# Kernel optimization log

Hardware: AMD Instinct MI355X
Metric: run time of the kernel (lower is better)

## Reference

```python
import jax, jax.numpy as jnp
import numpy as np

N = 50000   # nodes
E = 400000  # directed edges (line-graph nodes)
LE = 1600000  # line-graph edges
B = 256     # graphs in batch
F = 64      # n_feats
ED = 16     # edge_dim
NIT = 3     # n_iter
SF = 6 * F  # LinearBlock hidden


def _seg_softmax(vals, seg, num):
    # numerically stable segment softmax (PyG softmax)
    m = jax.ops.segment_max(vals, seg, num_segments=num)
    e = jnp.exp(vals - m[seg])
    s = jax.ops.segment_sum(e, seg, num_segments=num)
    return e / (s[seg] + 1e-16)


def _gat_pool(out, lg_src, lg_dst, batch, gat_W, att_src, att_dst, gat_bias):
    # PyG GATConv(F, 1): heads=1, add_self_loops=True, negative_slope=0.2
    xw = out @ gat_W                       # [E, 1]
    sl = jnp.arange(E, dtype=lg_src.dtype)
    src = jnp.concatenate([lg_src, sl])
    dst = jnp.concatenate([lg_dst, sl])
    a_s = xw[:, 0] * att_src[0]
    a_d = xw[:, 0] * att_dst[0]
    alpha = jax.nn.leaky_relu(a_s[src] + a_d[dst], negative_slope=0.2)
    coef = _seg_softmax(alpha, dst, E)     # softmax over incoming line-edges
    xc = jax.ops.segment_sum(coef[:, None] * xw[src], dst, num_segments=E) + gat_bias  # [E,1]
    # GlobalAttentionPool: segment softmax over batch, then weighted sum pool
    sc = _seg_softmax(xc[:, 0], batch, B)[:, None]
    return jax.ops.segment_sum(out * sc, batch, num_segments=B)  # [B, F]


def _bn(x, g, b):
    # BatchNorm1d in training mode (batch stats, biased var, eps=1e-5)
    m = x.mean(0)
    v = ((x - m) ** 2).mean(0)
    return (x - m) * jax.lax.rsqrt(v + 1e-5) * g + b


def _prelu(x, w):
    return jnp.where(x >= 0, x, w * x)


def _lin_block(x, bn1_g, bn1_b, W1, b1, bn_g, bn_b, pr, W, b, bn5_g, bn5_b, pr5, W5, b5):
    x = _bn(x, bn1_g, bn1_b) @ W1 + b1                       # lin1: [N, 6F]
    h = _prelu(_bn(x, bn_g[0], bn_b[0]), pr[0]) @ W[0] + b[0]  # lin2
    h = _prelu(_bn(h, bn_g[1], bn_b[1]), pr[1]) @ W[1] + b[1]  # lin3
    x = (h + x) / 2
    x = (_prelu(_bn(x, bn_g[2], bn_b[2]), pr[2]) @ W[2] + b[2] + x) / 2  # lin4
    x = _prelu(_bn(x, bn5_g, bn5_b), pr5) @ W5 + b5          # lin5: [N, F]
    return x


def setup_inputs() -> dict:
    key = jax.random.key(0)
    ks = jax.random.split(key, 20)
    def nrm(k, shape, s=0.1):
        return jax.random.normal(k, shape, jnp.float32) * s
    inp = {}
    inp["x"] = jax.random.normal(ks[0], (N, F), jnp.float32)
    inp["edge_attr"] = jax.random.normal(ks[1], (E, ED), jnp.float32)
    inp["edge_index"] = jax.random.randint(ks[2], (2, E), 0, N, jnp.int32)
    inp["line_graph_edge_index"] = jax.random.randint(ks[3], (2, LE), 0, E, jnp.int32)
    inp["edge_index_batch"] = jnp.sort(jax.random.randint(ks[4], (E,), 0, B, jnp.int32))
    inp["W_u"] = nrm(ks[5], (F, F)); inp["W_v"] = nrm(ks[6], (F, F)); inp["W_e"] = nrm(ks[7], (ED, F))
    inp["gat_W"] = nrm(ks[8], (F, 1)); inp["gat_att_src"] = nrm(ks[9], (1,)); inp["gat_att_dst"] = nrm(ks[10], (1,))
    inp["gat_bias"] = jnp.zeros((1,), jnp.float32)
    inp["a"] = nrm(ks[11], (1, F, NIT)); inp["a_bias"] = jnp.zeros((1, 1, NIT), jnp.float32)
    inp["W_gout"] = nrm(ks[12], (F, F)); inp["b_gout"] = jnp.zeros((F,), jnp.float32)
    inp["lb_bn1_g"] = jnp.ones((F,), jnp.float32); inp["lb_bn1_b"] = jnp.zeros((F,), jnp.float32)
    inp["lb_W1"] = nrm(ks[13], (F, SF)); inp["lb_b1"] = jnp.zeros((SF,), jnp.float32)
    inp["lb_bn_g"] = jnp.ones((3, SF), jnp.float32); inp["lb_bn_b"] = jnp.zeros((3, SF), jnp.float32)
    inp["lb_pr"] = jnp.full((3,), 0.25, jnp.float32)
    inp["lb_W"] = nrm(ks[14], (3, SF, SF)); inp["lb_b"] = jnp.zeros((3, SF), jnp.float32)
    inp["lb_bn5_g"] = jnp.ones((SF,), jnp.float32); inp["lb_bn5_b"] = jnp.zeros((SF,), jnp.float32)
    inp["lb_pr5"] = jnp.array(0.25, jnp.float32)
    inp["lb_W5"] = nrm(ks[15], (SF, F)); inp["lb_b5"] = jnp.zeros((F,), jnp.float32)
    return inp


def reference(x, edge_attr, W_u, W_v, W_e, gat_W, gat_att_src, gat_att_dst, gat_bias,
              a, a_bias, W_gout, b_gout,
              lb_bn1_g, lb_bn1_b, lb_W1, lb_b1, lb_bn_g, lb_bn_b, lb_pr, lb_W, lb_b,
              lb_bn5_g, lb_bn5_b, lb_pr5, lb_W5, lb_b5,
              edge_index, line_graph_edge_index, edge_index_batch):
    ei0, ei1 = edge_index[0], edge_index[1]
    lg0, lg1 = line_graph_edge_index[0], line_graph_edge_index[1]
    # initial directed-edge features
    ea = ((x @ W_u)[ei0] + (x @ W_v)[ei1] + edge_attr @ W_e) / 3.0  # [E, F]
    out = ea
    outs, gouts = [], []
    for _ in range(NIT):
        out = ea + jax.ops.segment_sum(out[lg0], lg1, num_segments=E)  # line-graph message passing
        gout = _gat_pool(out, lg0, lg1, edge_index_batch, gat_W, gat_att_src, gat_att_dst, gat_bias)
        outs.append(out)
        gouts.append(jnp.tanh(gout @ W_gout + b_gout))
    out_all = jnp.stack(outs, -1)    # [E, F, NIT]
    gout_all = jnp.stack(gouts, -1)  # [B, F, NIT]
    sc = jax.nn.softmax((gout_all * a).sum(1, keepdims=True) + a_bias, axis=-1)  # [B,1,NIT]
    out = (out_all * sc[edge_index_batch]).sum(-1)  # per-edge gather == repeat_interleave(degree)
    xn = x + jax.ops.segment_sum(out, ei1, num_segments=N)
    return _lin_block(xn, lb_bn1_g, lb_bn1_b, lb_W1, lb_b1, lb_bn_g, lb_bn_b, lb_pr, lb_W, lb_b,
                      lb_bn5_g, lb_bn5_b, lb_pr5, lb_W5, lb_b5)
```

## Files before the change

### kernel.cpp

```cpp
#include <hip/hip_runtime.h>
#include <math.h>

#define NN 50000
#define EE 400000
#define LEE 1600000
#define BBATCH 256
#define FF 64
#define EDD 16
#define NITER 3
#define SFD 384

#define CDIV(a,b) (((a)+(b)-1)/(b))

typedef unsigned short ushort_t;
typedef __attribute__((ext_vector_type(8))) short bf16x8;
typedef __attribute__((ext_vector_type(4))) float f32x4;

__device__ inline float b2f(ushort_t u) { return __uint_as_float(((unsigned)u) << 16); }
__device__ inline ushort_t f2b(float f) {
    unsigned u = __float_as_uint(f);
    return (ushort_t)((u + 0x7fffu + ((u >> 16) & 1u)) >> 16);
}

__global__ void k_hist(const int* __restrict__ idx, int n, int* __restrict__ cnt) {
    int i = blockIdx.x * blockDim.x + threadIdx.x;
    if (i < n) atomicAdd(&cnt[idx[i]], 1);
}
__global__ void k_part(const int* __restrict__ in, int n, int* __restrict__ part) {
    __shared__ int s[256];
    int i = blockIdx.x * 256 + threadIdx.x;
    s[threadIdx.x] = (i < n) ? in[i] : 0;
    __syncthreads();
    for (int off = 128; off > 0; off >>= 1) {
        if (threadIdx.x < off) s[threadIdx.x] += s[threadIdx.x + off];
        __syncthreads();
    }
    if (threadIdx.x == 0) part[blockIdx.x] = s[0];
}
__global__ void k_scan_single(int* __restrict__ a, int n) {
    __shared__ int s[256];
    int v = (threadIdx.x < n) ? a[threadIdx.x] : 0;
    s[threadIdx.x] = v; __syncthreads();
    for (int off = 1; off < 256; off <<= 1) {
        int t = (threadIdx.x >= off) ? s[threadIdx.x - off] : 0;
        __syncthreads(); s[threadIdx.x] += t; __syncthreads();
    }
    if (threadIdx.x < n) a[threadIdx.x] = s[threadIdx.x] - v;
}
__global__ void k_scan_add(int* __restrict__ a, int n, const int* __restrict__ off) {
    __shared__ int s[256];
    int i = blockIdx.x * 256 + threadIdx.x;
    int v = (i < n) ? a[i] : 0;
    s[threadIdx.x] = v; __syncthreads();
    for (int o = 1; o < 256; o <<= 1) {
        int t = (threadIdx.x >= o) ? s[threadIdx.x - o] : 0;
        __syncthreads(); s[threadIdx.x] += t; __syncthreads();
    }
    if (i < n) a[i] = s[threadIdx.x] - v + off[blockIdx.x];
}
__global__ void k_scan_out(const int* __restrict__ in, int n, const int* __restrict__ boff,
                           int* __restrict__ out) {
    __shared__ int s[256];
    int i = blockIdx.x * 256 + threadIdx.x;
    int v = (i < n) ? in[i] : 0;
    s[threadIdx.x] = v; __syncthreads();
    for (int o = 1; o < 256; o <<= 1) {
        int t = (threadIdx.x >= o) ? s[threadIdx.x - o] : 0;
        __syncthreads(); s[threadIdx.x] += t; __syncthreads();
    }
    if (i < n) out[i] = s[threadIdx.x] - v + boff[blockIdx.x];
    if (i == n - 1) out[n] = s[threadIdx.x] + boff[blockIdx.x];
}
__global__ void k_fill_lg(const int* __restrict__ lg, const int* __restrict__ rowptr,
                          int* __restrict__ cnt, int* __restrict__ srcidx) {
    int i = blockIdx.x * blockDim.x + threadIdx.x;
    if (i >= LEE) return;
    int d = lg[LEE + i];
    int pos = rowptr[d] + atomicAdd(&cnt[d], 1);
    srcidx[pos] = lg[i];
}
__global__ void k_fill_n(const int* __restrict__ ei, const int* __restrict__ rowptr,
                         int* __restrict__ cnt, int* __restrict__ nidx) {
    int i = blockIdx.x * blockDim.x + threadIdx.x;
    if (i >= EE) return;
    int d = ei[EE + i];
    int pos = rowptr[d] + atomicAdd(&cnt[d], 1);
    nidx[pos] = i;
}


__global__ void k_node_mm(const float* __restrict__ x, const float* __restrict__ Wu,
                          const float* __restrict__ Wv, ushort_t* __restrict__ xu,
                          ushort_t* __restrict__ xv) {
    __shared__ float su[64 * 64];
    __shared__ float sv[64 * 64];
    int tid = threadIdx.x;
    for (int i = tid; i < 64 * 64; i += blockDim.x) { su[i] = Wu[i]; sv[i] = Wv[i]; }
    __syncthreads();
    int row = blockIdx.x * 4 + (tid >> 6);
    int f = tid & 63;
    if (row >= NN) return;
    const float* xr = x + (long long)row * 64;
    float au = 0.f, av = 0.f;
    #pragma unroll
    for (int k = 0; k < 64; ++k) {
        float xv_ = xr[k];
        au += xv_ * su[k * 64 + f];
        av += xv_ * sv[k * 64 + f];
    }
    xu[(long long)row * 64 + f] = f2b(au);
    xv[(long long)row * 64 + f] = f2b(av);
}

__global__ void k_ea_b16(const ushort_t* __restrict__ xu, const ushort_t* __restrict__ xv,
                         const float* __restrict__ eattr, const float* __restrict__ We,
                         const int* __restrict__ ei, ushort_t* __restrict__ eab) {
    __shared__ float swe[16 * 64];
    int tid = threadIdx.x;
    for (int i = tid; i < 1024; i += 256) swe[i] = We[i];
    __syncthreads();
    int e = blockIdx.x * 8 + (tid >> 5);
    int f2 = (tid & 31) * 2;
    if (e >= EE) return;
    int s = ei[e];
    int d = ei[EE + e];
    unsigned us = *(const unsigned*)&xu[(long long)s * 64 + f2];
    unsigned ud = *(const unsigned*)&xv[(long long)d * 64 + f2];
    const float* ar = eattr + (long long)e * 16;
    float a0 = 0.f, a1 = 0.f;
    #pragma unroll
    for (int k = 0; k < 16; ++k) {
        float w = ar[k];
        a0 += w * swe[k * 64 + f2];
        a1 += w * swe[k * 64 + f2 + 1];
    }
    float v0 = (b2f((ushort_t)us) + b2f((ushort_t)ud) + a0) * (1.0f / 3.0f);
    float v1 = (b2f((ushort_t)(us >> 16)) + b2f((ushort_t)(ud >> 16)) + a1) * (1.0f / 3.0f);
    *(unsigned*)&eab[(long long)e * 64 + f2] = (unsigned)f2b(v0) | ((unsigned)f2b(v1) << 16);
}

__global__ void k_mp_gather(const ushort_t* __restrict__ prev,
                            const ushort_t* __restrict__ eab,
                            const int* __restrict__ rowptr, const int* __restrict__ srcidx,
                            const float* __restrict__ gatW,
                            ushort_t* __restrict__ outb, float* __restrict__ xw) {
    int tid = threadIdx.x;
    int d = blockIdx.x * 8 + (tid >> 5);
    int f2 = (tid & 31) * 2;
    if (d >= EE) return;
    unsigned ue = *(const unsigned*)&eab[(long long)d * 64 + f2];
    float a0 = b2f((ushort_t)ue), a1 = b2f((ushort_t)(ue >> 16));
    int p0 = rowptr[d], p1 = rowptr[d + 1];
    int j = p0;
    for (; j + 4 <= p1; j += 4) {
        int s0 = srcidx[j], s1 = srcidx[j + 1], s2 = srcidx[j + 2], s3 = srcidx[j + 3];
        unsigned u0 = *(const unsigned*)&prev[(long long)s0 * 64 + f2];
        unsigned u1 = *(const unsigned*)&prev[(long long)s1 * 64 + f2];
        unsigned u2 = *(const unsigned*)&prev[(long long)s2 * 64 + f2];
        unsigned u3 = *(const unsigned*)&prev[(long long)s3 * 64 + f2];
        a0 += (b2f((ushort_t)u0) + b2f((ushort_t)u1)) + (b2f((ushort_t)u2) + b2f((ushort_t)u3));
        a1 += (b2f((ushort_t)(u0 >> 16)) + b2f((ushort_t)(u1 >> 16))) +
              (b2f((ushort_t)(u2 >> 16)) + b2f((ushort_t)(u3 >> 16)));
    }
    for (; j < p1; ++j) {
        unsigned u0 = *(const unsigned*)&prev[(long long)srcidx[j] * 64 + f2];
        a0 += b2f((ushort_t)u0);
        a1 += b2f((ushort_t)(u0 >> 16));
    }
    *(unsigned*)&outb[(long long)d * 64 + f2] = (unsigned)f2b(a0) | ((unsigned)f2b(a1) << 16);
    float w = a0 * gatW[f2] + a1 * gatW[f2 + 1];
    #pragma unroll
    for (int o = 16; o > 0; o >>= 1) w += __shfl_down(w, o, 32);
    if ((tid & 31) == 0) xw[d] = w;
}

__global__ void k_gat_fused(const float* __restrict__ xw,
                            const int* __restrict__ rowptr, const int* __restrict__ srcidx,
                            const float* __restrict__ att_s, const float* __restrict__ att_d,
                            const float* __restrict__ gbias, float* __restrict__ xc) {
    int e = blockIdx.x * blockDim.x + threadIdx.x;
    if (e >= EE) return;
    float as = att_s[0], ad = att_d[0];
    float xwd = xw[e];
    float adt = xwd * ad;
    float aself = xwd * as + adt;
    if (aself < 0.f) aself *= 0.2f;
    int p0 = rowptr[e], p1 = rowptr[e + 1];
    float m = aself;
    for (int j = p0; j < p1; ++j) {
        float a = xw[srcidx[j]] * as + adt;
        if (a < 0.f) a *= 0.2f;
        m = fmaxf(m, a);
    }
    float ssum = expf(aself - m);
    float wsum = ssum * xwd;
    for (int j = p0; j < p1; ++j) {
        float xs = xw[srcidx[j]];
        float a = xs * as + adt;
        if (a < 0.f) a *= 0.2f;
        float ev = expf(a - m);
        ssum += ev;
        wsum += ev * xs;
    }
    xc[e] = wsum / (ssum + 1e-16f) + gbias[0];
}

__global__ void k_batchptr(const int* __restrict__ batch, int* __restrict__ bptr) {
    int e = blockIdx.x * blockDim.x + threadIdx.x;
    if (e >= EE) return;
    int b = batch[e];
    int bp = (e == 0) ? -1 : batch[e - 1];
    for (int q = bp + 1; q <= b; ++q) bptr[q] = e;
    if (e == EE - 1)
        for (int q = b + 1; q <= BBATCH; ++q) bptr[q] = EE;
}

__global__ void k_pool(const float* __restrict__ xc, const ushort_t* __restrict__ out,
                       const int* __restrict__ bptr, float* __restrict__ gout) {
    int b = blockIdx.x;
    int p0 = bptr[b], p1 = bptr[b + 1];
    __shared__ float red[256];
    int tid = threadIdx.x;
    float mx = -INFINITY;
    for (int e = p0 + tid; e < p1; e += 256) mx = fmaxf(mx, xc[e]);
    red[tid] = mx; __syncthreads();
    for (int s = 128; s > 0; s >>= 1) { if (tid < s) red[tid] = fmaxf(red[tid], red[tid + s]); __syncthreads(); }
    float m = red[0]; __syncthreads();
    float sm = 0.f;
    for (int e = p0 + tid; e < p1; e += 256) sm += expf(xc[e] - m);
    red[tid] = sm; __syncthreads();
    for (int s = 128; s > 0; s >>= 1) { if (tid < s) red[tid] += red[tid + s]; __syncthreads(); }
    float ssum = red[0] + 1e-16f; __syncthreads();
    int f = tid & 63, chunk = tid >> 6;
    float acc = 0.f;
    for (int e = p0 + chunk; e < p1; e += 4) {
        float w = expf(xc[e] - m);
        acc += w * b2f(out[(long long)e * 64 + f]);
    }
    red[tid] = acc; __syncthreads();
    if (chunk == 0) {
        float tot = red[f] + red[64 + f] + red[128 + f] + red[192 + f];
        gout[b * 64 + f] = tot / ssum;
    }
}

__global__ void k_gout_mm(const float* __restrict__ gout, const float* __restrict__ Wg,
                          const float* __restrict__ bg, float* __restrict__ gt) {
    __shared__ float sw[64 * 64];
    int tid = threadIdx.x;
    for (int i = tid; i < 4096; i += blockDim.x) sw[i] = Wg[i];
    __syncthreads();
    int row = blockIdx.x * 4 + (tid >> 6);
    int f = tid & 63;
    if (row >= BBATCH) return;
    const float* gr = gout + row * 64;
    float acc = bg[f];
    #pragma unroll
    for (int k = 0; k < 64; ++k) acc += gr[k] * sw[k * 64 + f];
    gt[row * 64 + f] = tanhf(acc);
}

__global__ void k_att(const float* __restrict__ g0, const float* __restrict__ g1,
                      const float* __restrict__ g2, const float* __restrict__ a,
                      const float* __restrict__ abias, float* __restrict__ sc) {
    int b = blockIdx.x;
    int f = threadIdx.x;
    float v0 = g0[b * 64 + f] * a[f * 3 + 0];
    float v1 = g1[b * 64 + f] * a[f * 3 + 1];
    float v2 = g2[b * 64 + f] * a[f * 3 + 2];
    #pragma unroll
    for (int o = 32; o > 0; o >>= 1) {
        v0 += __shfl_down(v0, o, 64);
        v1 += __shfl_down(v1, o, 64);
        v2 += __shfl_down(v2, o, 64);
    }
    if (f == 0) {
        float s0 = v0 + abias[0], s1 = v1 + abias[1], s2 = v2 + abias[2];
        float m = fmaxf(s0, fmaxf(s1, s2));
        float e0 = expf(s0 - m), e1 = expf(s1 - m), e2 = expf(s2 - m);
        float inv = 1.0f / (e0 + e1 + e2);
        sc[b * 3 + 0] = e0 * inv; sc[b * 3 + 1] = e1 * inv; sc[b * 3 + 2] = e2 * inv;
    }
}

__global__ void k_comb(ushort_t* __restrict__ o1, const ushort_t* __restrict__ o2,
                       const ushort_t* __restrict__ o3, const float* __restrict__ sc,
                       const int* __restrict__ batch) {
    long long idx = (long long)blockIdx.x * blockDim.x + threadIdx.x;
    if (idx >= (long long)EE * 64) return;
    int e = (int)(idx >> 6);
    int b = batch[e];
    float v = b2f(o1[idx]) * sc[b * 3] + b2f(o2[idx]) * sc[b * 3 + 1] + b2f(o3[idx]) * sc[b * 3 + 2];
    o1[idx] = f2b(v);
}

__global__ void k_node_gather(const ushort_t* __restrict__ comb, const int* __restrict__ nrow,
                              const int* __restrict__ nidx, const float* __restrict__ x,
                              ushort_t* __restrict__ xnb) {
    int tid = threadIdx.x;
    int n = blockIdx.x * 4 + (tid >> 6);
    int f = tid & 63;
    if (n >= NN) return;
    float acc = x[(long long)n * 64 + f];
    int p0 = nrow[n], p1 = nrow[n + 1];
    int j = p0;
    for (; j + 4 <= p1; j += 4) {
        int e0 = nidx[j], e1 = nidx[j + 1], e2 = nidx[j + 2], e3 = nidx[j + 3];
        float v0 = b2f(comb[(long long)e0 * 64 + f]);
        float v1 = b2f(comb[(long long)e1 * 64 + f]);
        float v2 = b2f(comb[(long long)e2 * 64 + f]);
        float v3 = b2f(comb[(long long)e3 * 64 + f]);
        acc += (v0 + v1) + (v2 + v3);
    }
    for (; j < p1; ++j) acc += b2f(comb[(long long)nidx[j] * 64 + f]);
    xnb[(long long)n * 64 + f] = f2b(acc);
}

__global__ void k_colstats_b16(const ushort_t* __restrict__ X, int ncols, int nrows,
                               float* __restrict__ csum, float* __restrict__ csumsq) {
    int c = threadIdx.x;
    int rpb = CDIV(nrows, (int)gridDim.x);
    int r0 = blockIdx.x * rpb;
    int r1 = min(r0 + rpb, nrows);
    float s = 0.f, s2 = 0.f;
    for (int r = r0; r < r1; ++r) {
        float v = b2f(X[(long long)r * ncols + c]);
        s += v; s2 += v * v;
    }
    atomicAdd(&csum[c], s);
    atomicAdd(&csumsq[c], s2);
}

template<int MT>
__global__ __launch_bounds__(512) void k_gemm_lb(
    const ushort_t* __restrict__ A, const float* __restrict__ W,
    const float* __restrict__ bias, const ushort_t* __restrict__ resb,
    const float* __restrict__ csum, const float* __restrict__ csumsq,
    const float* __restrict__ g, const float* __restrict__ bb,
    const float* __restrict__ pr, float scale, int nrows, int K,
    ushort_t* __restrict__ Cb, float* __restrict__ Cf,
    float* __restrict__ osum, float* __restrict__ osumsq) {
    constexpr int NF = MT / 32;
    __shared__ ushort_t sA[64][40];
    __shared__ ushort_t sB[MT][40];
    __shared__ float sScl[SFD], sOff[SFD];
    int tid = threadIdx.x;
    int wave = tid >> 6, lane = tid & 63;
    int l16 = lane & 15, klo = lane >> 4;
    int rowg = wave >> 1, colg = wave & 1;
    long long rowBase = (long long)blockIdx.x * 64;
    float prs = pr ? pr[0] : 1.0f;
    const float invn = 1.0f / (float)NN;
    for (int c = tid; c < K; c += 512) {
        float mean = csum[c] * invn;
        float var = csumsq[c] * invn - mean * mean;
        float scl = rsqrtf(var + 1e-5f) * g[c];
        sScl[c] = scl;
        sOff[c] = bb[c] - mean * scl;
    }
    __syncthreads();
    f32x4 acc[NF] = {};
    for (int k0 = 0; k0 < K; k0 += 32) {
        {
            int i4 = tid * 4;
            int r = i4 >> 5, kk = i4 & 31;
            long long gr = rowBase + r;
            unsigned lo = 0, hi = 0;
            if (gr < nrows) {
                const ushort_t* ap = &A[gr * K + k0 + kk];
                unsigned raw0 = *(const unsigned*)ap;
                unsigned raw1 = *(const unsigned*)(ap + 2);
                float t0 = b2f((ushort_t)raw0) * sScl[k0 + kk] + sOff[k0 + kk];
                float t1 = b2f((ushort_t)(raw0 >> 16)) * sScl[k0 + kk + 1] + sOff[k0 + kk + 1];
                float t2 = b2f((ushort_t)raw1) * sScl[k0 + kk + 2] + sOff[k0 + kk + 2];
                float t3 = b2f((ushort_t)(raw1 >> 16)) * sScl[k0 + kk + 3] + sOff[k0 + kk + 3];
                if (t0 < 0.f) t0 *= prs;
                if (t1 < 0.f) t1 *= prs;
                if (t2 < 0.f) t2 *= prs;
                if (t3 < 0.f) t3 *= prs;
                lo = (unsigned)f2b(t0) | ((unsigned)f2b(t1) << 16);
                hi = (unsigned)f2b(t2) | ((unsigned)f2b(t3) << 16);
            }
            uint2 pk; pk.x = lo; pk.y = hi;
            *(uint2*)&sA[r][kk] = pk;
        }
        for (int i = tid; i < 32 * MT; i += 512) {
            int col = i % MT, kk = i / MT;
            sB[col][kk] = f2b(W[(long long)(k0 + kk) * MT + col]);
        }
        __syncthreads();
        bf16x8 af = *(const bf16x8*)&sA[rowg * 16 + l16][klo * 8];
        #pragma unroll
        for (int n = 0; n < NF; ++n) {
            bf16x8 bf = *(const bf16x8*)&sB[colg * (MT / 2) + n * 16 + l16][klo * 8];
            acc[n] = __builtin_amdgcn_mfma_f32_16x16x32_bf16(af, bf, acc[n], 0, 0, 0);
        }
        __syncthreads();
    }
    #pragma unroll
    for (int n = 0; n < NF; ++n) {
        int col = colg * (MT / 2) + n * 16 + l16;
        long long row0 = rowBase + rowg * 16 + klo * 4;
        float bcol = bias[col];
        float s = 0.f, s2 = 0.f;
        #pragma unroll
        for (int r = 0; r < 4; ++r) {
            long long row = row0 + r;
            if (row < nrows) {
                float v = acc[n][r] + bcol;
                if (resb) v += b2f(resb[row * MT + col]);
                v *= scale;
                if (Cf) Cf[row * MT + col] = v;
                if (Cb) Cb[row * MT + col] = f2b(v);
                s += v; s2 += v * v;
            }
        }
        if (osum) {
            s += __shfl_down(s, 32, 64);
            s2 += __shfl_down(s2, 32, 64);
            s += __shfl_down(s, 16, 64);
            s2 += __shfl_down(s2, 16, 64);
            if (lane < 16) {
                atomicAdd(&osum[col], s);
                atomicAdd(&osumsq[col], s2);
            }
        }
    }
}

extern "C" void kernel_launch(void* const* d_in, const int* in_sizes, int n_in,
                              void* d_out, int out_size, void* d_ws, size_t ws_size,
                              hipStream_t stream) {
    const float* x       = (const float*)d_in[0];
    const float* eattr   = (const float*)d_in[1];
    const int*   ei      = (const int*)d_in[2];
    const int*   lg      = (const int*)d_in[3];
    const int*   batch   = (const int*)d_in[4];
    const float* W_u     = (const float*)d_in[5];
    const float* W_v     = (const float*)d_in[6];
    const float* W_e     = (const float*)d_in[7];
    const float* gat_W   = (const float*)d_in[8];
    const float* att_s   = (const float*)d_in[9];
    const float* att_d   = (const float*)d_in[10];
    const float* gat_b   = (const float*)d_in[11];
    const float* a_att   = (const float*)d_in[12];
    const float* a_bias  = (const float*)d_in[13];
    const float* W_gout  = (const float*)d_in[14];
    const float* b_gout  = (const float*)d_in[15];
    const float* bn1_g   = (const float*)d_in[16];
    const float* bn1_b   = (const float*)d_in[17];
    const float* lb_W1   = (const float*)d_in[18];
    const float* lb_b1   = (const float*)d_in[19];
    const float* lb_bn_g = (const float*)d_in[20];
    const float* lb_bn_b = (const float*)d_in[21];
    const float* lb_pr   = (const float*)d_in[22];
    const float* lb_W    = (const float*)d_in[23];
    const float* lb_b    = (const float*)d_in[24];
    const float* bn5_g   = (const float*)d_in[25];
    const float* bn5_b   = (const float*)d_in[26];
    const float* pr5     = (const float*)d_in[27];
    const float* lb_W5   = (const float*)d_in[28];
    const float* lb_b5   = (const float*)d_in[29];
    float* out_final = (float*)d_out;

    const long long ESZ = (long long)EE * FF;
    const long long NSZ = (long long)NN * FF;
    char* cur = (char*)d_ws;
    auto alloc = [&](size_t bytes) -> void* {
        void* p = (void*)cur;
        cur += (bytes + 255) & ~(size_t)255;
        return p;
    };
    ushort_t* XU = (ushort_t*)alloc(NSZ * 2);
    ushort_t* XV = (ushort_t*)alloc(NSZ * 2);
    ushort_t* O1 = (ushort_t*)alloc(ESZ * 2);
    ushort_t* O2 = (ushort_t*)alloc(ESZ * 2);
    ushort_t* O3 = (ushort_t*)alloc(ESZ * 2);
    float* XW = (float*)alloc((size_t)EE * 4);
    float* XC = (float*)alloc((size_t)EE * 4);
    ushort_t* XNB = (ushort_t*)alloc(NSZ * 2);
    float* GRAW = (float*)alloc(BBATCH * FF * 4);
    float* G0 = (float*)alloc(BBATCH * FF * 4);
    float* G1 = (float*)alloc(BBATCH * FF * 4);
    float* G2 = (float*)alloc(BBATCH * FF * 4);
    float* SCATT = (float*)alloc(BBATCH * 3 * 4);
    int* BPTR = (int*)alloc((BBATCH + 1) * 4);
    int* LROW = (int*)alloc((size_t)(EE + 1) * 4);
    int* LSRC = (int*)alloc((size_t)LEE * 4);
    int* LCNT = (int*)alloc((size_t)EE * 4);
    int* NROW = (int*)alloc((size_t)(NN + 1) * 4);
    int* NIDX = (int*)alloc((size_t)EE * 4);
    int* NCNT = (int*)alloc((size_t)NN * 4);
    int* SP0 = (int*)alloc(2048 * 4);
    int* SP1 = (int*)alloc(256 * 4);
    float* STATS = (float*)alloc(5 * 2 * SFD * 4);
    if ((size_t)(cur - (char*)d_ws) > ws_size) return;

    ushort_t* T1B = O1;
    ushort_t* T2B = T1B + (long long)NN * SFD;
    ushort_t* T3B = T2B + (long long)NN * SFD;
    ushort_t* T4B = T3B + (long long)NN * SFD;
    float* CS[5][2];
    for (int i = 0; i < 5; ++i) { CS[i][0] = STATS + i * 2 * SFD; CS[i][1] = CS[i][0] + SFD; }
    float* GTS[3] = {G0, G1, G2};

    hipMemsetAsync(STATS, 0, 5 * 2 * SFD * 4, stream);

    k_node_mm<<<CDIV(NN, 4), 256, 0, stream>>>(x, W_u, W_v, XU, XV);
    k_batchptr<<<CDIV(EE, 256), 256, 0, stream>>>(batch, BPTR);

    {
        hipMemsetAsync(LCNT, 0, (size_t)EE * 4, stream);
        k_hist<<<CDIV(LEE, 256), 256, 0, stream>>>(lg + LEE, LEE, LCNT);
        int nb0 = CDIV(EE, 256), nb1 = CDIV(nb0, 256);
        k_part<<<nb0, 256, 0, stream>>>(LCNT, EE, SP0);
        k_part<<<nb1, 256, 0, stream>>>(SP0, nb0, SP1);
        k_scan_single<<<1, 256, 0, stream>>>(SP1, nb1);
        k_scan_add<<<nb1, 256, 0, stream>>>(SP0, nb0, SP1);
        k_scan_out<<<nb0, 256, 0, stream>>>(LCNT, EE, SP0, LROW);
        hipMemsetAsync(LCNT, 0, (size_t)EE * 4, stream);
        k_fill_lg<<<CDIV(LEE, 256), 256, 0, stream>>>(lg, LROW, LCNT, LSRC);
    }
    {
        hipMemsetAsync(NCNT, 0, (size_t)NN * 4, stream);
        k_hist<<<CDIV(EE, 256), 256, 0, stream>>>(ei + EE, EE, NCNT);
        int nb0 = CDIV(NN, 256), nb1 = CDIV(nb0, 256);
        k_part<<<nb0, 256, 0, stream>>>(NCNT, NN, SP0);
        k_part<<<nb1, 256, 0, stream>>>(SP0, nb0, SP1);
        k_scan_single<<<1, 256, 0, stream>>>(SP1, nb1);
        k_scan_add<<<nb1, 256, 0, stream>>>(SP0, nb0, SP1);
        k_scan_out<<<nb0, 256, 0, stream>>>(NCNT, NN, SP0, NROW);
        hipMemsetAsync(NCNT, 0, (size_t)NN * 4, stream);
        k_fill_n<<<CDIV(EE, 256), 256, 0, stream>>>(ei, NROW, NCNT, NIDX);
    }

    const int EB8 = CDIV(EE, 8);

    auto gat_pool = [&](ushort_t* buf, int t) {
        k_gat_fused<<<CDIV(EE, 256), 256, 0, stream>>>(XW, LROW, LSRC, att_s, att_d, gat_b, XC);
        k_pool<<<BBATCH, 256, 0, stream>>>(XC, buf, BPTR, GRAW);
        k_gout_mm<<<CDIV(BBATCH, 4), 256, 0, stream>>>(GRAW, W_gout, b_gout, GTS[t]);
    };

    k_ea_b16<<<EB8, 256, 0, stream>>>(XU, XV, eattr, W_e, ei, O3);
    k_mp_gather<<<EB8, 256, 0, stream>>>(O3, O3, LROW, LSRC, gat_W, O1, XW);
    gat_pool(O1, 0);
    k_mp_gather<<<EB8, 256, 0, stream>>>(O1, O3, LROW, LSRC, gat_W, O2, XW);
    gat_pool(O2, 1);
    k_mp_gather<<<EB8, 256, 0, stream>>>(O2, O3, LROW, LSRC, gat_W, O3, XW);
    gat_pool(O3, 2);

    k_att<<<BBATCH, 64, 0, stream>>>(G0, G1, G2, a_att, a_bias, SCATT);
    k_comb<<<(int)CDIV(ESZ, 256), 256, 0, stream>>>(O1, O2, O3, SCATT, batch);
    k_node_gather<<<CDIV(NN, 4), 256, 0, stream>>>(O1, NROW, NIDX, x, XNB);
    k_colstats_b16<<<256, FF, 0, stream>>>(XNB, FF, NN, CS[0][0], CS[0][1]);

    const int GB = CDIV(NN, 64);
    k_gemm_lb<384><<<GB, 512, 0, stream>>>(XNB, lb_W1, lb_b1, nullptr,
        CS[0][0], CS[0][1], bn1_g, bn1_b, nullptr, 1.0f, NN, FF,
        T1B, nullptr, CS[1][0], CS[1][1]);
    k_gemm_lb<384><<<GB, 512, 0, stream>>>(T1B, lb_W, lb_b, nullptr,
        CS[1][0], CS[1][1], lb_bn_g, lb_bn_b, lb_pr, 1.0f, NN, SFD,
        T2B, nullptr, CS[2][0], CS[2][1]);
    k_gemm_lb<384><<<GB, 512, 0, stream>>>(T2B, lb_W + (long long)SFD * SFD, lb_b + SFD, T1B,
        CS[2][0], CS[2][1], lb_bn_g + SFD, lb_bn_b + SFD, lb_pr + 1, 0.5f, NN, SFD,
        T3B, nullptr, CS[3][0], CS[3][1]);
    k_gemm_lb<384><<<GB, 512, 0, stream>>>(T3B, lb_W + 2LL * SFD * SFD, lb_b + 2 * SFD, T3B,
        CS[3][0], CS[3][1], lb_bn_g + 2 * SFD, lb_bn_b + 2 * SFD, lb_pr + 2, 0.5f, NN, SFD,
        T4B, nullptr, CS[4][0], CS[4][1]);
    k_gemm_lb<64><<<GB, 512, 0, stream>>>(T4B, lb_W5, lb_b5, nullptr,
        CS[4][0], CS[4][1], bn5_g, bn5_b, pr5, 1.0f, NN, SFD,
        nullptr, out_final, nullptr, nullptr);
}
```

Before: 2.204 ms.

## Retile LinearBlock GEMMs with pre-transposed bf16 weights and 64x64 per-wave tiles

Pre-transposes and converts the LinearBlock weight matrices to bf16 once, in a small kernel. The GEMMs now use 128x128 (or 256x64) block tiles with each wave computing a 4x4 grid of MFMA tiles, and B fragments are read directly from global memory. This removes the per-k-step fp32-to-bf16 weight conversion into shared memory and raises MFMA reuse per A load. The cost is more register pressure and B reads that are uncached global loads rather than shared-memory staged.

```diff
diff --git a/kernel.cpp b/kernel.cpp
--- a/kernel.cpp
+++ b/kernel.cpp
@@ -331,27 +331,42 @@
     atomicAdd(&csumsq[c], s2);
 }
 
-template<int MT>
-__global__ __launch_bounds__(512) void k_gemm_lb(
-    const ushort_t* __restrict__ A, const float* __restrict__ W,
+__global__ void k_wtrans(const float* __restrict__ W, int K, int M, ushort_t* __restrict__ Wt) {
+    __shared__ ushort_t tile[32][33];
+    int kb = blockIdx.y * 32, mb = blockIdx.x * 32;
+    int tx = threadIdx.x & 31, ty = threadIdx.x >> 5;
+    for (int dy = ty; dy < 32; dy += 8) {
+        int k = kb + dy, m = mb + tx;
+        tile[dy][tx] = (k < K && m < M) ? f2b(W[(long long)k * M + m]) : (ushort_t)0;
+    }
+    __syncthreads();
+    for (int dy = ty; dy < 32; dy += 8) {
+        int m = mb + dy, k = kb + tx;
+        if (m < M && k < K) Wt[(long long)m * K + k] = tile[tx][dy];
+    }
+}
+
+template<int KK, int WR, int WC>
+__global__ __launch_bounds__(256) void k_gemm_fused(
+    const ushort_t* __restrict__ A, const ushort_t* __restrict__ Wt,
     const float* __restrict__ bias, const ushort_t* __restrict__ resb,
     const float* __restrict__ csum, const float* __restrict__ csumsq,
     const float* __restrict__ g, const float* __restrict__ bb,
-    const float* __restrict__ pr, float scale, int nrows, int K,
+    const float* __restrict__ pr, float scale, int nrows, int M,
     ushort_t* __restrict__ Cb, float* __restrict__ Cf,
     float* __restrict__ osum, float* __restrict__ osumsq) {
-    constexpr int NF = MT / 32;
-    __shared__ ushort_t sA[64][40];
-    __shared__ ushort_t sB[MT][40];
-    __shared__ float sScl[SFD], sOff[SFD];
+    constexpr int RT = WR * 64;
+    __shared__ ushort_t sA[RT][36];
+    __shared__ float sScl[KK], sOff[KK];
     int tid = threadIdx.x;
     int wave = tid >> 6, lane = tid & 63;
     int l16 = lane & 15, klo = lane >> 4;
-    int rowg = wave >> 1, colg = wave & 1;
-    long long rowBase = (long long)blockIdx.x * 64;
+    int wrow = wave / WC, wcol = wave % WC;
+    long long rowBase = (long long)blockIdx.x * RT;
+    int colBase = blockIdx.y * (WC * 64);
     float prs = pr ? pr[0] : 1.0f;
     const float invn = 1.0f / (float)NN;
-    for (int c = tid; c < K; c += 512) {
+    for (int c = tid; c < KK; c += 256) {
         float mean = csum[c] * invn;
         float var = csumsq[c] * invn - mean * mean;
         float scl = rsqrtf(var + 1e-5f) * g[c];
@@ -359,70 +374,83 @@
         sOff[c] = bb[c] - mean * scl;
     }
     __syncthreads();
-    f32x4 acc[NF] = {};
-    for (int k0 = 0; k0 < K; k0 += 32) {
-        {
-            int i4 = tid * 4;
-            int r = i4 >> 5, kk = i4 & 31;
+    f32x4 acc[4][4] = {};
+    for (int k0 = 0; k0 < KK; k0 += 32) {
+        #pragma unroll
+        for (int it = 0; it < RT * 32 / (256 * 8); ++it) {
+            int idx = (it * 256 + tid) * 8;
+            int r = idx >> 5, kk = idx & 31;
             long long gr = rowBase + r;
-            unsigned lo = 0, hi = 0;
-            if (gr < nrows) {
-                const ushort_t* ap = &A[gr * K + k0 + kk];
-                unsigned raw0 = *(const unsigned*)ap;
-                unsigned raw1 = *(const unsigned*)(ap + 2);
-                float t0 = b2f((ushort_t)raw0) * sScl[k0 + kk] + sOff[k0 + kk];
-                float t1 = b2f((ushort_t)(raw0 >> 16)) * sScl[k0 + kk + 1] + sOff[k0 + kk + 1];
-                float t2 = b2f((ushort_t)raw1) * sScl[k0 + kk + 2] + sOff[k0 + kk + 2];
-                float t3 = b2f((ushort_t)(raw1 >> 16)) * sScl[k0 + kk + 3] + sOff[k0 + kk + 3];
+            uint4 raw = {0u, 0u, 0u, 0u};
+            if (gr < nrows) raw = *(const uint4*)&A[gr * KK + k0 + kk];
+            unsigned outw[4];
+            #pragma unroll
+            for (int q = 0; q < 4; ++q) {
+                unsigned rw = ((const unsigned*)&raw)[q];
+                int c = k0 + kk + q * 2;
+                float t0 = b2f((ushort_t)rw) * sScl[c] + sOff[c];
+                float t1 = b2f((ushort_t)(rw >> 16)) * sScl[c + 1] + sOff[c + 1];
                 if (t0 < 0.f) t0 *= prs;
                 if (t1 < 0.f) t1 *= prs;
-                if (t2 < 0.f) t2 *= prs;
-                if (t3 < 0.f) t3 *= prs;
-                lo = (unsigned)f2b(t0) | ((unsigned)f2b(t1) << 16);
-                hi = (unsigned)f2b(t2) | ((unsigned)f2b(t3) << 16);
+                outw[q] = (unsigned)f2b(t0) | ((unsigned)f2b(t1) << 16);
             }
-            uint2 pk; pk.x = lo; pk.y = hi;
-            *(uint2*)&sA[r][kk] = pk;
-        }
-        for (int i = tid; i < 32 * MT; i += 512) {
-            int col = i % MT, kk = i / MT;
-            sB[col][kk] = f2b(W[(long long)(k0 + kk) * MT + col]);
+            uint2 w0; w0.x = outw[0]; w0.y = outw[1];
+            uint2 w1; w1.x = outw[2]; w1.y = outw[3];
+            *(uint2*)&sA[r][kk] = w0;
+            *(uint2*)&sA[r][kk + 4] = w1;
         }
         __syncthreads();
-        bf16x8 af = *(const bf16x8*)&sA[rowg * 16 + l16][klo * 8];
+        bf16x8 bfr[4];
         #pragma unroll
-        for (int n = 0; n < NF; ++n) {
-            bf16x8 bf = *(const bf16x8*)&sB[colg * (MT / 2) + n * 16 + l16][klo * 8];
-            acc[n] = __builtin_amdgcn_mfma_f32_16x16x32_bf16(af, bf, acc[n], 0, 0, 0);
+        for (int n = 0; n < 4; ++n) {
+            int col = colBase + wcol * 64 + n * 16 + l16;
+            bfr[n] = *(const bf16x8*)&Wt[(long long)col * KK + k0 + klo * 8];
         }
+        bf16x8 afr[4];
+        #pragma unroll
+        for (int m = 0; m < 4; ++m) {
+            union { uint2 p[2]; bf16x8 v; } u;
+            int row = wrow * 64 + m * 16 + l16;
+            u.p[0] = *(const uint2*)&sA[row][klo * 8];
+            u.p[1] = *(const uint2*)&sA[row][klo * 8 + 4];
+            afr[m] = u.v;
+        }
+        #pragma unroll
+        for (int m = 0; m < 4; ++m)
+            #pragma unroll
+            for (int n = 0; n < 4; ++n)
+                acc[m][n] = __builtin_amdgcn_mfma_f32_16x16x32_bf16(afr[m], bfr[n], acc[m][n], 0, 0, 0);
         __syncthreads();
     }
     #pragma unroll
-    for (int n = 0; n < NF; ++n) {
-        int col = colg * (MT / 2) + n * 16 + l16;
-        long long row0 = rowBase + rowg * 16 + klo * 4;
-        float bcol = bias[col];
-        float s = 0.f, s2 = 0.f;
+    for (int m = 0; m < 4; ++m) {
         #pragma unroll
-        for (int r = 0; r < 4; ++r) {
-            long long row = row0 + r;
-            if (row < nrows) {
-                float v = acc[n][r] + bcol;
-                if (resb) v += b2f(resb[row * MT + col]);
-                v *= scale;
-                if (Cf) Cf[row * MT + col] = v;
-                if (Cb) Cb[row * MT + col] = f2b(v);
-                s += v; s2 += v * v;
+        for (int n = 0; n < 4; ++n) {
+            int col = colBase + wcol * 64 + n * 16 + l16;
+            long long row0 = rowBase + wrow * 64 + m * 16 + klo * 4;
+            float bcol = bias[col];
+            float s = 0.f, s2 = 0.f;
+            #pragma unroll
+            for (int r = 0; r < 4; ++r) {
+                long long row = row0 + r;
+                if (row < nrows) {
+                    float v = acc[m][n][r] + bcol;
+                    if (resb) v += b2f(resb[row * M + col]);
+                    v *= scale;
+                    if (Cf) Cf[row * M + col] = v;
+                    if (Cb) Cb[row * M + col] = f2b(v);
+                    s += v; s2 += v * v;
+                }
             }
-        }
-        if (osum) {
-            s += __shfl_down(s, 32, 64);
-            s2 += __shfl_down(s2, 32, 64);
-            s += __shfl_down(s, 16, 64);
-            s2 += __shfl_down(s2, 16, 64);
-            if (lane < 16) {
-                atomicAdd(&osum[col], s);
-                atomicAdd(&osumsq[col], s2);
+            if (osum) {
+                s += __shfl_down(s, 32, 64);
+                s2 += __shfl_down(s2, 32, 64);
+                s += __shfl_down(s, 16, 64);
+                s2 += __shfl_down(s2, 16, 64);
+                if (lane < 16) {
+                    atomicAdd(&osum[col], s);
+                    atomicAdd(&osumsq[col], s2);
+                }
             }
         }
     }
@@ -494,6 +522,11 @@
     int* SP0 = (int*)alloc(2048 * 4);
     int* SP1 = (int*)alloc(256 * 4);
     float* STATS = (float*)alloc(5 * 2 * SFD * 4);
+    ushort_t* WT1 = (ushort_t*)alloc((size_t)SFD * FF * 2);
+    ushort_t* WT2 = (ushort_t*)alloc((size_t)SFD * SFD * 2);
+    ushort_t* WT3 = (ushort_t*)alloc((size_t)SFD * SFD * 2);
+    ushort_t* WT4 = (ushort_t*)alloc((size_t)SFD * SFD * 2);
+    ushort_t* WT5 = (ushort_t*)alloc((size_t)FF * SFD * 2);
     if ((size_t)(cur - (char*)d_ws) > ws_size) return;
 
     ushort_t* T1B = O1;
@@ -505,6 +538,17 @@
     float* GTS[3] = {G0, G1, G2};
 
     hipMemsetAsync(STATS, 0, 5 * 2 * SFD * 4, stream);
+
+    {
+        dim3 gt(SFD / 32, FF / 32);
+        k_wtrans<<<gt, 256, 0, stream>>>(lb_W1, FF, SFD, WT1);
+        dim3 gs(SFD / 32, SFD / 32);
+        k_wtrans<<<gs, 256, 0, stream>>>(lb_W, SFD, SFD, WT2);
+        k_wtrans<<<gs, 256, 0, stream>>>(lb_W + (long long)SFD * SFD, SFD, SFD, WT3);
+        k_wtrans<<<gs, 256, 0, stream>>>(lb_W + 2LL * SFD * SFD, SFD, SFD, WT4);
+        dim3 g5(FF / 32, SFD / 32);
+        k_wtrans<<<g5, 256, 0, stream>>>(lb_W5, SFD, FF, WT5);
+    }
 
     k_node_mm<<<CDIV(NN, 4), 256, 0, stream>>>(x, W_u, W_v, XU, XV);
     k_batchptr<<<CDIV(EE, 256), 256, 0, stream>>>(batch, BPTR);
@@ -555,20 +599,23 @@
     k_node_gather<<<CDIV(NN, 4), 256, 0, stream>>>(O1, NROW, NIDX, x, XNB);
     k_colstats_b16<<<256, FF, 0, stream>>>(XNB, FF, NN, CS[0][0], CS[0][1]);
 
-    const int GB = CDIV(NN, 64);
-    k_gemm_lb<384><<<GB, 512, 0, stream>>>(XNB, lb_W1, lb_b1, nullptr,
-        CS[0][0], CS[0][1], bn1_g, bn1_b, nullptr, 1.0f, NN, FF,
-        T1B, nullptr, CS[1][0], CS[1][1]);
-    k_gemm_lb<384><<<GB, 512, 0, stream>>>(T1B, lb_W, lb_b, nullptr,
-        CS[1][0], CS[1][1], lb_bn_g, lb_bn_b, lb_pr, 1.0f, NN, SFD,
-        T2B, nullptr, CS[2][0], CS[2][1]);
-    k_gemm_lb<384><<<GB, 512, 0, stream>>>(T2B, lb_W + (long long)SFD * SFD, lb_b + SFD, T1B,
-        CS[2][0], CS[2][1], lb_bn_g + SFD, lb_bn_b + SFD, lb_pr + 1, 0.5f, NN, SFD,
-        T3B, nullptr, CS[3][0], CS[3][1]);
-    k_gemm_lb<384><<<GB, 512, 0, stream>>>(T3B, lb_W + 2LL * SFD * SFD, lb_b + 2 * SFD, T3B,
-        CS[3][0], CS[3][1], lb_bn_g + 2 * SFD, lb_bn_b + 2 * SFD, lb_pr + 2, 0.5f, NN, SFD,
-        T4B, nullptr, CS[4][0], CS[4][1]);
-    k_gemm_lb<64><<<GB, 512, 0, stream>>>(T4B, lb_W5, lb_b5, nullptr,
-        CS[4][0], CS[4][1], bn5_g, bn5_b, pr5, 1.0f, NN, SFD,
-        nullptr, out_final, nullptr, nullptr);
-}
+    {
+        dim3 g(CDIV(NN, 128), SFD / 128);
+        k_gemm_fused<64, 2, 2><<<g, 256, 0, stream>>>(XNB, WT1, lb_b1, nullptr,
+            CS[0][0], CS[0][1], bn1_g, bn1_b, nullptr, 1.0f, NN, SFD,
+            T1B, nullptr, CS[1][0], CS[1][1]);
+        k_gemm_fused<384, 2, 2><<<g, 256, 0, stream>>>(T1B, WT2, lb_b, nullptr,
+            CS[1][0], CS[1][1], lb_bn_g, lb_bn_b, lb_pr, 1.0f, NN, SFD,
+            T2B, nullptr, CS[2][0], CS[2][1]);
+        k_gemm_fused<384, 2, 2><<<g, 256, 0, stream>>>(T2B, WT3, lb_b + SFD, T1B,
+            CS[2][0], CS[2][1], lb_bn_g + SFD, lb_bn_b + SFD, lb_pr + 1, 0.5f, NN, SFD,
+            T3B, nullptr, CS[3][0], CS[3][1]);
+        k_gemm_fused<384, 2, 2><<<g, 256, 0, stream>>>(T3B, WT4, lb_b + 2 * SFD, T3B,
+            CS[3][0], CS[3][1], lb_bn_g + 2 * SFD, lb_bn_b + 2 * SFD, lb_pr + 2, 0.5f, NN, SFD,
+            T4B, nullptr, CS[4][0], CS[4][1]);
+        dim3 g5(CDIV(NN, 256), 1);
+        k_gemm_fused<384, 4, 1><<<g5, 256, 0, stream>>>(T4B, WT5, lb_b5, nullptr,
+            CS[4][0], CS[4][1], bn5_g, bn5_b, pr5, 1.0f, NN, FF,
+            nullptr, out_final, nullptr, nullptr);
+    }
+}
```

New measurement: 2.082 ms. -5.5%, faster.
